# Optimization experiments

Hardware: AMD Instinct MI355X
Metric: run time of the kernel (lower is better)

Reference implementation:

```python
import jax, jax.numpy as jnp
import numpy as np

B, N, D, C, TOPK = 64, 2048, 512, 128, 8
LN_EPS = 1e-5


def setup_inputs() -> dict:
    key = jax.random.key(0)
    k_x, k_len, k_y, k_w, k_b = jax.random.split(key, 5)
    x = jax.random.normal(k_x, (B, N, D), dtype=jnp.float32)
    # per-sample valid lengths in [TOPK, N] -> prefix mask (every sample has >= TOPK valid clips)
    lengths = jax.random.randint(k_len, (B,), TOPK, N + 1)
    mask = jnp.arange(N)[None, :] < lengths[:, None]  # (B, N) bool
    y = jax.random.randint(k_y, (B,), 0, C)
    ln_w = jnp.ones((D,), dtype=jnp.float32)
    ln_b = jnp.zeros((D,), dtype=jnp.float32)
    W = jax.random.normal(k_w, (D, C), dtype=jnp.float32) / np.sqrt(D)
    b = jax.random.normal(k_b, (C,), dtype=jnp.float32) * 0.01
    return {"x": x, "ln_w": ln_w, "ln_b": ln_b, "W": W, "b": b, "mask": mask, "y": y}


def reference(x, ln_w, ln_b, W, b, mask, y):
    # LayerNorm over last dim
    mu = jnp.mean(x, axis=-1, keepdims=True)
    var = jnp.mean(jnp.square(x - mu), axis=-1, keepdims=True)
    xn = (x - mu) * jax.lax.rsqrt(var + LN_EPS) * ln_w + ln_b  # (B,N,D)
    # per-clip logits
    clip_logits = jnp.einsum('bnd,dc->bnc', xn, W) + b  # (B,N,C)
    # score at ground-truth class, invalid clips -> -inf
    score = jnp.take_along_axis(clip_logits, y[:, None, None], axis=2)[..., 0]  # (B,N)
    score = jnp.where(mask, score, -jnp.inf)
    # batched top-k (k fixed; masks guarantee >= TOPK valid entries)
    _, idx = jax.lax.top_k(score, TOPK)  # (B,TOPK)
    sel = jnp.take_along_axis(clip_logits, idx[:, :, None], axis=1)  # (B,TOPK,C)
    logits = jnp.mean(sel, axis=1)  # (B,C)
    return logits
```

## Files before the change

### kernel.cpp

```cpp
#include <hip/hip_runtime.h>
#include <math.h>

#define B_    64
#define N_    2048
#define D_    512
#define C_    128
#define TOPK_ 8
#define LN_EPS_ 1e-5f

__global__ __launch_bounds__(256) void prep_kernel(
    const float* __restrict__ ln_w, const float* __restrict__ ln_b,
    const float* __restrict__ W, const float* __restrict__ bias,
    const int* __restrict__ y, const unsigned char* __restrict__ mask,
    float* __restrict__ cw, float* __restrict__ cb, float* __restrict__ su,
    int* __restrict__ len) {
  int b = blockIdx.x;
  int t = threadIdx.x;
  int cls = y[b];
  __shared__ float red0[256];
  __shared__ float red1[256];
  __shared__ int   red2[256];
  float l0 = 0.f, l1 = 0.f;
  for (int d = t; d < D_; d += 256) {
    float wcol = W[d * C_ + cls];
    float u = ln_w[d] * wcol;
    cw[b * D_ + d] = u;
    l0 += ln_b[d] * wcol;
    l1 += u;
  }
  int cnt = 0;
  unsigned int tag = *(const unsigned int*)mask;
  if (tag == 1u) {
    const int* m32 = (const int*)mask;
    for (int i = t; i < N_; i += 256) cnt += (m32[b * N_ + i] != 0);
  } else if (tag == 0x01010101u) {
    for (int i = t; i < N_; i += 256) cnt += (mask[b * N_ + i] != 0);
  } else {
    const float* mf = (const float*)mask;
    for (int i = t; i < N_; i += 256) cnt += (mf[b * N_ + i] != 0.f);
  }
  red0[t] = l0; red1[t] = l1; red2[t] = cnt;
  __syncthreads();
  for (int s = 128; s > 0; s >>= 1) {
    if (t < s) {
      red0[t] += red0[t + s];
      red1[t] += red1[t + s];
      red2[t] += red2[t + s];
    }
    __syncthreads();
  }
  if (t == 0) {
    cb[b] = red0[0] + bias[cls];
    su[b] = red1[0];
    len[b] = red2[0];
  }
}

__global__ __launch_bounds__(256) void score_kernel(
    const float* __restrict__ x, const float* __restrict__ cw,
    const float* __restrict__ cb, const float* __restrict__ su,
    const int* __restrict__ len, float* __restrict__ score) {
  int t = threadIdx.x;
  int wave = t >> 6;
  int lane = t & 63;
  int lg   = lane & 15;
  int g    = lane >> 4;
  int blk_clip0 = blockIdx.x * 16;
  int b    = blk_clip0 >> 11;
  int nblk = blk_clip0 & (N_ - 1);
  int L = len[b];

  __shared__ float4 cw_s[D_ / 4];

  if (nblk >= L) {
    if (t < 16) score[blk_clip0 + t] = -INFINITY;
    return;
  }
  if (t < 128) cw_s[t] = ((const float4*)(cw + (size_t)b * D_))[t];
  __syncthreads();

  int clip0 = blk_clip0 + wave * 4;
  int n0 = clip0 & (N_ - 1);
  if (n0 >= L) {
    if (lane < 4) score[clip0 + lane] = -INFINITY;
    return;
  }

  int cg = clip0 + g;
  const float4* xg = (const float4*)(x + (size_t)cg * D_);
  float4 xv[8];
  #pragma unroll
  for (int j = 0; j < 8; ++j) xv[j] = xg[j * 16 + lg];

  float s = 0.f, sq = 0.f, dt = 0.f;
  #pragma unroll
  for (int j = 0; j < 8; ++j) {
    float4 u = cw_s[j * 16 + lg];
    float4 a = xv[j];
    s  += a.x + a.y + a.z + a.w;
    sq  = fmaf(a.x, a.x, fmaf(a.y, a.y, fmaf(a.z, a.z, fmaf(a.w, a.w, sq))));
    dt  = fmaf(a.x, u.x, fmaf(a.y, u.y, fmaf(a.z, u.z, fmaf(a.w, u.w, dt))));
  }
  #pragma unroll
  for (int off = 1; off < 16; off <<= 1) {
    s  += __shfl_xor(s,  off);
    sq += __shfl_xor(sq, off);
    dt += __shfl_xor(dt, off);
  }
  if (lg == 0) {
    float mu = s * (1.f / D_);
    float var = sq * (1.f / D_) - mu * mu;
    float rstd = rsqrtf(var + LN_EPS_);
    float val = rstd * (dt - mu * su[b]) + cb[b];
    score[cg] = (n0 + g < L) ? val : -INFINITY;
  }
}

__global__ __launch_bounds__(128) void tail_kernel(
    const float* __restrict__ x, const float* __restrict__ ln_w,
    const float* __restrict__ ln_b, const float* __restrict__ W,
    const float* __restrict__ bias, const float* __restrict__ score,
    float* __restrict__ out) {
  int b = blockIdx.x >> 3;
  int k = blockIdx.x & 7;
  int t = threadIdx.x;
  int lane = t & 63;

  __shared__ int   top_s[TOPK_];
  __shared__ float xn_s[D_];
  __shared__ float red_s[2][2];

  if (t < 64) {
    float v[32];
    #pragma unroll
    for (int j = 0; j < 32; ++j) v[j] = score[b * N_ + j * 64 + lane];
    for (int k2 = 0; k2 < TOPK_; ++k2) {
      float bv = -INFINITY;
      int bi = N_;
      #pragma unroll
      for (int j = 0; j < 32; ++j) {
        int e = j * 64 + lane;
        if (v[j] > bv || (v[j] == bv && e < bi)) { bv = v[j]; bi = e; }
      }
      for (int off = 32; off > 0; off >>= 1) {
        float ov = __shfl_xor(bv, off);
        int   oi = __shfl_xor(bi, off);
        if (ov > bv || (ov == bv && oi < bi)) { bv = ov; bi = oi; }
      }
      if (lane == 0) top_s[k2] = bi;
      if ((bi & 63) == lane) v[bi >> 6] = -INFINITY;
    }
  }
  __syncthreads();

  int n = top_s[k];
  const float4* xp4 = (const float4*)(x + ((size_t)b * N_ + n) * D_);
  float4 xv = xp4[t];
  float s  = xv.x + xv.y + xv.z + xv.w;
  float sq = fmaf(xv.x, xv.x, fmaf(xv.y, xv.y, fmaf(xv.z, xv.z, xv.w * xv.w)));
  for (int off = 32; off > 0; off >>= 1) {
    s  += __shfl_xor(s,  off);
    sq += __shfl_xor(sq, off);
  }
  if (lane == 0) { red_s[t >> 6][0] = s; red_s[t >> 6][1] = sq; }
  __syncthreads();
  float mu   = (red_s[0][0] + red_s[1][0]) * (1.f / D_);
  float var  = (red_s[0][1] + red_s[1][1]) * (1.f / D_) - mu * mu;
  float rstd = rsqrtf(var + LN_EPS_);
  float4 wv = ((const float4*)ln_w)[t];
  float4 bv = ((const float4*)ln_b)[t];
  float4 yv;
  yv.x = fmaf((xv.x - mu) * rstd, wv.x, bv.x);
  yv.y = fmaf((xv.y - mu) * rstd, wv.y, bv.y);
  yv.z = fmaf((xv.z - mu) * rstd, wv.z, bv.z);
  yv.w = fmaf((xv.w - mu) * rstd, wv.w, bv.w);
  ((float4*)xn_s)[t] = yv;
  __syncthreads();

  float a0 = 0.f, a1 = 0.f, a2 = 0.f, a3 = 0.f;
  #pragma unroll 4
  for (int ch = 0; ch < D_ / 4; ++ch) {
    float4 xn = ((const float4*)xn_s)[ch];
    a0 = fmaf(xn.x, W[(ch * 4 + 0) * C_ + t], a0);
    a1 = fmaf(xn.y, W[(ch * 4 + 1) * C_ + t], a1);
    a2 = fmaf(xn.z, W[(ch * 4 + 2) * C_ + t], a2);
    a3 = fmaf(xn.w, W[(ch * 4 + 3) * C_ + t], a3);
  }
  float dot = (a0 + a1) + (a2 + a3);
  atomicAdd(&out[b * C_ + t], (dot + bias[t]) * (1.f / TOPK_));
}

extern "C" void kernel_launch(void* const* d_in, const int* in_sizes, int n_in,
                              void* d_out, int out_size, void* d_ws, size_t ws_size,
                              hipStream_t stream) {
  const float* x    = (const float*)d_in[0];
  const float* ln_w = (const float*)d_in[1];
  const float* ln_b = (const float*)d_in[2];
  const float* W    = (const float*)d_in[3];
  const float* bias = (const float*)d_in[4];
  const unsigned char* mask = (const unsigned char*)d_in[5];
  const int* y      = (const int*)d_in[6];
  float* out = (float*)d_out;

  char* ws = (char*)d_ws;
  float* cw    = (float*)ws;  ws += (size_t)B_ * D_ * sizeof(float);
  float* cb    = (float*)ws;  ws += (size_t)B_ * sizeof(float);
  float* su    = (float*)ws;  ws += (size_t)B_ * sizeof(float);
  int*   len   = (int*)ws;    ws += (size_t)B_ * sizeof(int);
  float* score = (float*)ws;

  hipMemsetAsync(out, 0, (size_t)B_ * C_ * sizeof(float), stream);

  prep_kernel <<<B_, 256, 0, stream>>>(ln_w, ln_b, W, bias, y, mask, cw, cb, su, len);
  score_kernel<<<(B_ * N_) / 16, 256, 0, stream>>>(x, cw, cb, su, len, score);
  tail_kernel <<<B_ * TOPK_, 128, 0, stream>>>(x, ln_w, ln_b, W, bias, score, out);
}
```

Before: 63.70 us.

## Fuse prep, score, top-k and tail into one cooperative kernel

Replaces the memset and the three separate launches with a single cooperative kernel of 512 persistent blocks. Grid-wide syncs separate the phases: prep/zeroing, masked LN-score, per-sample top-k, and the gather-and-project tail. Each block now loops over 256 clips instead of launching one block per 16 clips. This removes launch gaps and inter-kernel overheads. In exchange it cuts the memory-level parallelism of the bandwidth-heavy score phase and adds three grid barriers.

```diff
diff --git a/kernel.cpp b/kernel.cpp
--- a/kernel.cpp
+++ b/kernel.cpp
@@ -1,5 +1,8 @@
 #include <hip/hip_runtime.h>
+#include <hip/hip_cooperative_groups.h>
 #include <math.h>
+
+namespace cg = cooperative_groups;
 
 #define B_    64
 #define N_    2048
@@ -7,134 +10,126 @@
 #define C_    128
 #define TOPK_ 8
 #define LN_EPS_ 1e-5f
-
-__global__ __launch_bounds__(256) void prep_kernel(
-    const float* __restrict__ ln_w, const float* __restrict__ ln_b,
-    const float* __restrict__ W, const float* __restrict__ bias,
-    const int* __restrict__ y, const unsigned char* __restrict__ mask,
+#define GRID_ 512
+
+__global__ __launch_bounds__(256, 2) void fused_kernel(
+    const float* __restrict__ x, const float* __restrict__ ln_w,
+    const float* __restrict__ ln_b, const float* __restrict__ W,
+    const float* __restrict__ bias, const unsigned char* __restrict__ mask,
+    const int* __restrict__ y,
     float* __restrict__ cw, float* __restrict__ cb, float* __restrict__ su,
-    int* __restrict__ len) {
-  int b = blockIdx.x;
-  int t = threadIdx.x;
-  int cls = y[b];
+    int* __restrict__ len, float* __restrict__ score, int* __restrict__ tidx,
+    float* __restrict__ out) {
+  cg::grid_group grid = cg::this_grid();
+  const int blk = blockIdx.x;
+  const int t = threadIdx.x;
+  const int wave = t >> 6;
+  const int lane = t & 63;
+
   __shared__ float red0[256];
   __shared__ float red1[256];
   __shared__ int   red2[256];
-  float l0 = 0.f, l1 = 0.f;
-  for (int d = t; d < D_; d += 256) {
-    float wcol = W[d * C_ + cls];
-    float u = ln_w[d] * wcol;
-    cw[b * D_ + d] = u;
-    l0 += ln_b[d] * wcol;
-    l1 += u;
-  }
-  int cnt = 0;
-  unsigned int tag = *(const unsigned int*)mask;
-  if (tag == 1u) {
-    const int* m32 = (const int*)mask;
-    for (int i = t; i < N_; i += 256) cnt += (m32[b * N_ + i] != 0);
-  } else if (tag == 0x01010101u) {
-    for (int i = t; i < N_; i += 256) cnt += (mask[b * N_ + i] != 0);
-  } else {
-    const float* mf = (const float*)mask;
-    for (int i = t; i < N_; i += 256) cnt += (mf[b * N_ + i] != 0.f);
-  }
-  red0[t] = l0; red1[t] = l1; red2[t] = cnt;
-  __syncthreads();
-  for (int s = 128; s > 0; s >>= 1) {
-    if (t < s) {
-      red0[t] += red0[t + s];
-      red1[t] += red1[t + s];
-      red2[t] += red2[t + s];
-    }
-    __syncthreads();
-  }
-  if (t == 0) {
-    cb[b] = red0[0] + bias[cls];
-    su[b] = red1[0];
-    len[b] = red2[0];
-  }
-}
-
-__global__ __launch_bounds__(256) void score_kernel(
-    const float* __restrict__ x, const float* __restrict__ cw,
-    const float* __restrict__ cb, const float* __restrict__ su,
-    const int* __restrict__ len, float* __restrict__ score) {
-  int t = threadIdx.x;
-  int wave = t >> 6;
-  int lane = t & 63;
-  int lg   = lane & 15;
-  int g    = lane >> 4;
-  int blk_clip0 = blockIdx.x * 16;
-  int b    = blk_clip0 >> 11;
-  int nblk = blk_clip0 & (N_ - 1);
-  int L = len[b];
-
   __shared__ float4 cw_s[D_ / 4];
-
-  if (nblk >= L) {
-    if (t < 16) score[blk_clip0 + t] = -INFINITY;
-    return;
-  }
-  if (t < 128) cw_s[t] = ((const float4*)(cw + (size_t)b * D_))[t];
-  __syncthreads();
-
-  int clip0 = blk_clip0 + wave * 4;
-  int n0 = clip0 & (N_ - 1);
-  if (n0 >= L) {
-    if (lane < 4) score[clip0 + lane] = -INFINITY;
-    return;
-  }
-
-  int cg = clip0 + g;
-  const float4* xg = (const float4*)(x + (size_t)cg * D_);
-  float4 xv[8];
-  #pragma unroll
-  for (int j = 0; j < 8; ++j) xv[j] = xg[j * 16 + lg];
-
-  float s = 0.f, sq = 0.f, dt = 0.f;
-  #pragma unroll
-  for (int j = 0; j < 8; ++j) {
-    float4 u = cw_s[j * 16 + lg];
-    float4 a = xv[j];
-    s  += a.x + a.y + a.z + a.w;
-    sq  = fmaf(a.x, a.x, fmaf(a.y, a.y, fmaf(a.z, a.z, fmaf(a.w, a.w, sq))));
-    dt  = fmaf(a.x, u.x, fmaf(a.y, u.y, fmaf(a.z, u.z, fmaf(a.w, u.w, dt))));
-  }
-  #pragma unroll
-  for (int off = 1; off < 16; off <<= 1) {
-    s  += __shfl_xor(s,  off);
-    sq += __shfl_xor(sq, off);
-    dt += __shfl_xor(dt, off);
-  }
-  if (lg == 0) {
-    float mu = s * (1.f / D_);
-    float var = sq * (1.f / D_) - mu * mu;
-    float rstd = rsqrtf(var + LN_EPS_);
-    float val = rstd * (dt - mu * su[b]) + cb[b];
-    score[cg] = (n0 + g < L) ? val : -INFINITY;
-  }
-}
-
-__global__ __launch_bounds__(128) void tail_kernel(
-    const float* __restrict__ x, const float* __restrict__ ln_w,
-    const float* __restrict__ ln_b, const float* __restrict__ W,
-    const float* __restrict__ bias, const float* __restrict__ score,
-    float* __restrict__ out) {
-  int b = blockIdx.x >> 3;
-  int k = blockIdx.x & 7;
-  int t = threadIdx.x;
-  int lane = t & 63;
-
-  __shared__ int   top_s[TOPK_];
-  __shared__ float xn_s[D_];
-  __shared__ float red_s[2][2];
-
-  if (t < 64) {
+  __shared__ float  xn_s[D_];
+  __shared__ float  red_s[2][2];
+
+  if (blk < B_) {
+    int b = blk;
+    int cls = y[b];
+    float l0 = 0.f, l1 = 0.f;
+    for (int d = t; d < D_; d += 256) {
+      float wcol = W[d * C_ + cls];
+      float u = ln_w[d] * wcol;
+      cw[b * D_ + d] = u;
+      l0 += ln_b[d] * wcol;
+      l1 += u;
+    }
+    int cnt = 0;
+    unsigned int tag = *(const unsigned int*)mask;
+    if (tag == 1u) {
+      const int* m32 = (const int*)mask;
+      for (int i = t; i < N_; i += 256) cnt += (m32[b * N_ + i] != 0);
+    } else if (tag == 0x01010101u) {
+      for (int i = t; i < N_; i += 256) cnt += (mask[b * N_ + i] != 0);
+    } else {
+      const float* mf = (const float*)mask;
+      for (int i = t; i < N_; i += 256) cnt += (mf[b * N_ + i] != 0.f);
+    }
+    red0[t] = l0; red1[t] = l1; red2[t] = cnt;
+    __syncthreads();
+    for (int s = 128; s > 0; s >>= 1) {
+      if (t < s) {
+        red0[t] += red0[t + s];
+        red1[t] += red1[t + s];
+        red2[t] += red2[t + s];
+      }
+      __syncthreads();
+    }
+    if (t == 0) {
+      cb[b] = red0[0] + bias[cls];
+      su[b] = red1[0];
+      len[b] = red2[0];
+    }
+    if (t < C_) out[b * C_ + t] = 0.f;
+  }
+  grid.sync();
+
+  {
+    int b = blk >> 3;
+    int nbase = (blk & 7) << 8;
+    int L = len[b];
+    int lg = lane & 15;
+    int g  = lane >> 4;
+
+    if (nbase < L) {
+      if (t < 128) cw_s[t] = ((const float4*)(cw + (size_t)b * D_))[t];
+    }
+    __syncthreads();
+
+    for (int it = 0; it < 16; ++it) {
+      int n0 = nbase + it * 16 + wave * 4;
+      int clip0 = (b << 11) + n0;
+      if (n0 >= L) {
+        if (lane < 4) score[clip0 + lane] = -INFINITY;
+      } else {
+        int cgc = clip0 + g;
+        const float4* xg = (const float4*)(x + (size_t)cgc * D_);
+        float4 xv[8];
+        #pragma unroll
+        for (int j = 0; j < 8; ++j) xv[j] = xg[j * 16 + lg];
+        float s = 0.f, sq = 0.f, dt = 0.f;
+        #pragma unroll
+        for (int j = 0; j < 8; ++j) {
+          float4 u = cw_s[j * 16 + lg];
+          float4 a = xv[j];
+          s += a.x + a.y + a.z + a.w;
+          sq = fmaf(a.x, a.x, fmaf(a.y, a.y, fmaf(a.z, a.z, fmaf(a.w, a.w, sq))));
+          dt = fmaf(a.x, u.x, fmaf(a.y, u.y, fmaf(a.z, u.z, fmaf(a.w, u.w, dt))));
+        }
+        #pragma unroll
+        for (int off = 1; off < 16; off <<= 1) {
+          s  += __shfl_xor(s,  off);
+          sq += __shfl_xor(sq, off);
+          dt += __shfl_xor(dt, off);
+        }
+        if (lg == 0) {
+          float mu = s * (1.f / D_);
+          float var = sq * (1.f / D_) - mu * mu;
+          float rstd = rsqrtf(var + LN_EPS_);
+          float val = rstd * (dt - mu * su[b]) + cb[b];
+          score[cgc] = (n0 + g < L) ? val : -INFINITY;
+        }
+      }
+    }
+  }
+  grid.sync();
+
+  if (blk < B_ && t < 64) {
+    int b = blk;
     float v[32];
     #pragma unroll
     for (int j = 0; j < 32; ++j) v[j] = score[b * N_ + j * 64 + lane];
-    for (int k2 = 0; k2 < TOPK_; ++k2) {
+    for (int k = 0; k < TOPK_; ++k) {
       float bv = -INFINITY;
       int bi = N_;
       #pragma unroll
@@ -147,47 +142,54 @@
         int   oi = __shfl_xor(bi, off);
         if (ov > bv || (ov == bv && oi < bi)) { bv = ov; bi = oi; }
       }
-      if (lane == 0) top_s[k2] = bi;
+      if (lane == 0) tidx[b * TOPK_ + k] = bi;
       if ((bi & 63) == lane) v[bi >> 6] = -INFINITY;
     }
   }
-  __syncthreads();
-
-  int n = top_s[k];
-  const float4* xp4 = (const float4*)(x + ((size_t)b * N_ + n) * D_);
-  float4 xv = xp4[t];
-  float s  = xv.x + xv.y + xv.z + xv.w;
-  float sq = fmaf(xv.x, xv.x, fmaf(xv.y, xv.y, fmaf(xv.z, xv.z, xv.w * xv.w)));
-  for (int off = 32; off > 0; off >>= 1) {
-    s  += __shfl_xor(s,  off);
-    sq += __shfl_xor(sq, off);
-  }
-  if (lane == 0) { red_s[t >> 6][0] = s; red_s[t >> 6][1] = sq; }
-  __syncthreads();
-  float mu   = (red_s[0][0] + red_s[1][0]) * (1.f / D_);
-  float var  = (red_s[0][1] + red_s[1][1]) * (1.f / D_) - mu * mu;
-  float rstd = rsqrtf(var + LN_EPS_);
-  float4 wv = ((const float4*)ln_w)[t];
-  float4 bv = ((const float4*)ln_b)[t];
-  float4 yv;
-  yv.x = fmaf((xv.x - mu) * rstd, wv.x, bv.x);
-  yv.y = fmaf((xv.y - mu) * rstd, wv.y, bv.y);
-  yv.z = fmaf((xv.z - mu) * rstd, wv.z, bv.z);
-  yv.w = fmaf((xv.w - mu) * rstd, wv.w, bv.w);
-  ((float4*)xn_s)[t] = yv;
-  __syncthreads();
-
-  float a0 = 0.f, a1 = 0.f, a2 = 0.f, a3 = 0.f;
-  #pragma unroll 4
-  for (int ch = 0; ch < D_ / 4; ++ch) {
-    float4 xn = ((const float4*)xn_s)[ch];
-    a0 = fmaf(xn.x, W[(ch * 4 + 0) * C_ + t], a0);
-    a1 = fmaf(xn.y, W[(ch * 4 + 1) * C_ + t], a1);
-    a2 = fmaf(xn.z, W[(ch * 4 + 2) * C_ + t], a2);
-    a3 = fmaf(xn.w, W[(ch * 4 + 3) * C_ + t], a3);
-  }
-  float dot = (a0 + a1) + (a2 + a3);
-  atomicAdd(&out[b * C_ + t], (dot + bias[t]) * (1.f / TOPK_));
+  grid.sync();
+
+  {
+    int b = blk >> 3;
+    int k = blk & 7;
+    int n = tidx[b * TOPK_ + k];
+    float4 xv = make_float4(0.f, 0.f, 0.f, 0.f);
+    if (t < 128) xv = ((const float4*)(x + ((size_t)b * N_ + n) * D_))[t];
+    float s  = xv.x + xv.y + xv.z + xv.w;
+    float sq = fmaf(xv.x, xv.x, fmaf(xv.y, xv.y, fmaf(xv.z, xv.z, xv.w * xv.w)));
+    for (int off = 32; off > 0; off >>= 1) {
+      s  += __shfl_xor(s,  off);
+      sq += __shfl_xor(sq, off);
+    }
+    if (lane == 0 && wave < 2) { red_s[wave][0] = s; red_s[wave][1] = sq; }
+    __syncthreads();
+    float mu   = (red_s[0][0] + red_s[1][0]) * (1.f / D_);
+    float var  = (red_s[0][1] + red_s[1][1]) * (1.f / D_) - mu * mu;
+    float rstd = rsqrtf(var + LN_EPS_);
+    if (t < 128) {
+      float4 wv = ((const float4*)ln_w)[t];
+      float4 bv = ((const float4*)ln_b)[t];
+      float4 yv;
+      yv.x = fmaf((xv.x - mu) * rstd, wv.x, bv.x);
+      yv.y = fmaf((xv.y - mu) * rstd, wv.y, bv.y);
+      yv.z = fmaf((xv.z - mu) * rstd, wv.z, bv.z);
+      yv.w = fmaf((xv.w - mu) * rstd, wv.w, bv.w);
+      ((float4*)xn_s)[t] = yv;
+    }
+    __syncthreads();
+    if (t < C_) {
+      float a0 = 0.f, a1 = 0.f, a2 = 0.f, a3 = 0.f;
+      #pragma unroll 4
+      for (int ch = 0; ch < D_ / 4; ++ch) {
+        float4 xn = ((const float4*)xn_s)[ch];
+        a0 = fmaf(xn.x, W[(ch * 4 + 0) * C_ + t], a0);
+        a1 = fmaf(xn.y, W[(ch * 4 + 1) * C_ + t], a1);
+        a2 = fmaf(xn.z, W[(ch * 4 + 2) * C_ + t], a2);
+        a3 = fmaf(xn.w, W[(ch * 4 + 3) * C_ + t], a3);
+      }
+      float dot = (a0 + a1) + (a2 + a3);
+      atomicAdd(&out[b * C_ + t], (dot + bias[t]) * (1.f / TOPK_));
+    }
+  }
 }
 
 extern "C" void kernel_launch(void* const* d_in, const int* in_sizes, int n_in,
@@ -207,11 +209,11 @@
   float* cb    = (float*)ws;  ws += (size_t)B_ * sizeof(float);
   float* su    = (float*)ws;  ws += (size_t)B_ * sizeof(float);
   int*   len   = (int*)ws;    ws += (size_t)B_ * sizeof(int);
-  float* score = (float*)ws;
-
-  hipMemsetAsync(out, 0, (size_t)B_ * C_ * sizeof(float), stream);
-
-  prep_kernel <<<B_, 256, 0, stream>>>(ln_w, ln_b, W, bias, y, mask, cw, cb, su, len);
-  score_kernel<<<(B_ * N_) / 16, 256, 0, stream>>>(x, cw, cb, su, len, score);
-  tail_kernel <<<B_ * TOPK_, 128, 0, stream>>>(x, ln_w, ln_b, W, bias, score, out);
+  float* score = (float*)ws;  ws += (size_t)B_ * N_ * sizeof(float);
+  int*   tidx  = (int*)ws;
+
+  void* args[] = {&x, &ln_w, &ln_b, &W, &bias, &mask, &y,
+                  &cw, &cb, &su, &len, &score, &tidx, &out};
+  hipLaunchCooperativeKernel(reinterpret_cast<const void*>(&fused_kernel),
+                             dim3(GRID_), dim3(256), args, 0, stream);
 }
```

New measurement: 224.1 us. 252% more time.

## Fuse prep kernel and output memset into score kernel

Applied to the files above, without the earlier changes.

Removes the separate prep kernel and the memset by having each score block recompute the class-column weights, bias term and sum for its sample into shared memory, and zero the output in the first blocks. Validity is read per clip from the mask instead of via a precomputed length, and blocks skip work when their first clip is invalid, which relies on the mask being a prefix. This saves two launches and their serialization but makes every valid block do strided reads of a W column (512 scattered loads) plus an extra reduction and barrier.

```diff
diff --git a/kernel.cpp b/kernel.cpp
--- a/kernel.cpp
+++ b/kernel.cpp
@@ -8,86 +8,63 @@
 #define TOPK_ 8
 #define LN_EPS_ 1e-5f
 
-__global__ __launch_bounds__(256) void prep_kernel(
-    const float* __restrict__ ln_w, const float* __restrict__ ln_b,
-    const float* __restrict__ W, const float* __restrict__ bias,
-    const int* __restrict__ y, const unsigned char* __restrict__ mask,
-    float* __restrict__ cw, float* __restrict__ cb, float* __restrict__ su,
-    int* __restrict__ len) {
-  int b = blockIdx.x;
-  int t = threadIdx.x;
+__global__ __launch_bounds__(256) void score_kernel(
+    const float* __restrict__ x, const float* __restrict__ ln_w,
+    const float* __restrict__ ln_b, const float* __restrict__ W,
+    const float* __restrict__ bias, const unsigned char* __restrict__ mask,
+    const int* __restrict__ y, float* __restrict__ score,
+    float* __restrict__ out) {
+  const int t = threadIdx.x;
+  const int wave = t >> 6;
+  const int lane = t & 63;
+  const int lg = lane & 15;
+  const int g  = lane >> 4;
+  const int blk_clip0 = blockIdx.x * 16;
+  const int b = blk_clip0 >> 11;
+
+  __shared__ float4 cw_s[D_ / 4];
+  __shared__ int    valid_s[16];
+  __shared__ float  part[4][2];
+
+  if (blockIdx.x < 32) out[blockIdx.x * 256 + t] = 0.f;
+
+  unsigned int tag = *(const unsigned int*)mask;
+  if (t < 16) {
+    int clip = blk_clip0 + t;
+    int v;
+    if (tag == 1u)               v = ((const int*)mask)[clip] != 0;
+    else if (tag == 0x01010101u) v = mask[clip] != 0;
+    else                         v = ((const float*)mask)[clip] != 0.f;
+    valid_s[t] = v;
+  }
+  __syncthreads();
+
+  if (!valid_s[0]) {
+    if (t < 16) score[blk_clip0 + t] = -INFINITY;
+    return;
+  }
+
   int cls = y[b];
-  __shared__ float red0[256];
-  __shared__ float red1[256];
-  __shared__ int   red2[256];
   float l0 = 0.f, l1 = 0.f;
   for (int d = t; d < D_; d += 256) {
     float wcol = W[d * C_ + cls];
     float u = ln_w[d] * wcol;
-    cw[b * D_ + d] = u;
+    ((float*)cw_s)[d] = u;
     l0 += ln_b[d] * wcol;
     l1 += u;
   }
-  int cnt = 0;
-  unsigned int tag = *(const unsigned int*)mask;
-  if (tag == 1u) {
-    const int* m32 = (const int*)mask;
-    for (int i = t; i < N_; i += 256) cnt += (m32[b * N_ + i] != 0);
-  } else if (tag == 0x01010101u) {
-    for (int i = t; i < N_; i += 256) cnt += (mask[b * N_ + i] != 0);
-  } else {
-    const float* mf = (const float*)mask;
-    for (int i = t; i < N_; i += 256) cnt += (mf[b * N_ + i] != 0.f);
+  #pragma unroll
+  for (int off = 32; off > 0; off >>= 1) {
+    l0 += __shfl_xor(l0, off);
+    l1 += __shfl_xor(l1, off);
   }
-  red0[t] = l0; red1[t] = l1; red2[t] = cnt;
+  if (lane == 0) { part[wave][0] = l0; part[wave][1] = l1; }
   __syncthreads();
-  for (int s = 128; s > 0; s >>= 1) {
-    if (t < s) {
-      red0[t] += red0[t + s];
-      red1[t] += red1[t + s];
-      red2[t] += red2[t + s];
-    }
-    __syncthreads();
-  }
-  if (t == 0) {
-    cb[b] = red0[0] + bias[cls];
-    su[b] = red1[0];
-    len[b] = red2[0];
-  }
-}
+  float cb_b = part[0][0] + part[1][0] + part[2][0] + part[3][0] + bias[cls];
+  float su_b = part[0][1] + part[1][1] + part[2][1] + part[3][1];
 
-__global__ __launch_bounds__(256) void score_kernel(
-    const float* __restrict__ x, const float* __restrict__ cw,
-    const float* __restrict__ cb, const float* __restrict__ su,
-    const int* __restrict__ len, float* __restrict__ score) {
-  int t = threadIdx.x;
-  int wave = t >> 6;
-  int lane = t & 63;
-  int lg   = lane & 15;
-  int g    = lane >> 4;
-  int blk_clip0 = blockIdx.x * 16;
-  int b    = blk_clip0 >> 11;
-  int nblk = blk_clip0 & (N_ - 1);
-  int L = len[b];
-
-  __shared__ float4 cw_s[D_ / 4];
-
-  if (nblk >= L) {
-    if (t < 16) score[blk_clip0 + t] = -INFINITY;
-    return;
-  }
-  if (t < 128) cw_s[t] = ((const float4*)(cw + (size_t)b * D_))[t];
-  __syncthreads();
-
-  int clip0 = blk_clip0 + wave * 4;
-  int n0 = clip0 & (N_ - 1);
-  if (n0 >= L) {
-    if (lane < 4) score[clip0 + lane] = -INFINITY;
-    return;
-  }
-
-  int cg = clip0 + g;
-  const float4* xg = (const float4*)(x + (size_t)cg * D_);
+  int cgc = blk_clip0 + wave * 4 + g;
+  const float4* xg = (const float4*)(x + (size_t)cgc * D_);
   float4 xv[8];
   #pragma unroll
   for (int j = 0; j < 8; ++j) xv[j] = xg[j * 16 + lg];
@@ -111,8 +88,8 @@
     float mu = s * (1.f / D_);
     float var = sq * (1.f / D_) - mu * mu;
     float rstd = rsqrtf(var + LN_EPS_);
-    float val = rstd * (dt - mu * su[b]) + cb[b];
-    score[cg] = (n0 + g < L) ? val : -INFINITY;
+    float val = rstd * (dt - mu * su_b) + cb_b;
+    score[cgc] = valid_s[wave * 4 + g] ? val : -INFINITY;
   }
 }
 
@@ -202,16 +179,10 @@
   const int* y      = (const int*)d_in[6];
   float* out = (float*)d_out;
 
-  char* ws = (char*)d_ws;
-  float* cw    = (float*)ws;  ws += (size_t)B_ * D_ * sizeof(float);
-  float* cb    = (float*)ws;  ws += (size_t)B_ * sizeof(float);
-  float* su    = (float*)ws;  ws += (size_t)B_ * sizeof(float);
-  int*   len   = (int*)ws;    ws += (size_t)B_ * sizeof(int);
-  float* score = (float*)ws;
+  float* score = (float*)d_ws;
 
-  hipMemsetAsync(out, 0, (size_t)B_ * C_ * sizeof(float), stream);
-
-  prep_kernel <<<B_, 256, 0, stream>>>(ln_w, ln_b, W, bias, y, mask, cw, cb, su, len);
-  score_kernel<<<(B_ * N_) / 16, 256, 0, stream>>>(x, cw, cb, su, len, score);
-  tail_kernel <<<B_ * TOPK_, 128, 0, stream>>>(x, ln_w, ln_b, W, bias, score, out);
+  score_kernel<<<(B_ * N_) / 16, 256, 0, stream>>>(
+      x, ln_w, ln_b, W, bias, mask, y, score, out);
+  tail_kernel <<<B_ * TOPK_, 128, 0, stream>>>(
+      x, ln_w, ln_b, W, bias, score, out);
 }
```

Result: faster. 52.10 us (-18.2%).
